# Optimization experiments

Measured on AMD Instinct MI355X. Metric: run time of the kernel, lower is better.

## Reference

```python
import jax, jax.numpy as jnp
import numpy as np

EPS = 1e-5
K_EDE, T_EDE = 1.0, 0.1  # IR-Net EDE STE params (init values); forward is pure sign


def binq(x):
    # sign binarization (forward only)
    return jnp.sign(x)


def conv3x3(x, w):
    return jax.lax.conv_general_dilated(
        x, w, window_strides=(1, 1), padding=[(1, 1), (1, 1)],
        dimension_numbers=("NCHW", "OIHW", "NCHW"))


def batchnorm(x, g, b):
    # training-mode BN: batch statistics over (N,H,W), biased variance
    mu = x.mean(axis=(0, 2, 3), keepdims=True)
    var = x.var(axis=(0, 2, 3), keepdims=True)
    return (x - mu) * jax.lax.rsqrt(var + EPS) * g.reshape(1, -1, 1, 1) + b.reshape(1, -1, 1, 1)


def maxpool2(x):
    return jax.lax.reduce_window(x, -jnp.inf, jax.lax.max,
                                 (1, 1, 2, 2), (1, 1, 2, 2), "VALID")


def hardtanh(x):
    return jnp.clip(x, -1.0, 1.0)


def skd_ir_conv(xb, xr, w):
    # IR-Net style 1W1A conv: per-out-channel standardize weights, sign-binarize
    # weights and activations; real branch uses full-precision weights, no grad.
    m = w.mean(axis=(1, 2, 3), keepdims=True)
    s = w.std(axis=(1, 2, 3), keepdims=True, ddof=1)  # torch std is unbiased
    bw = binq((w - m) / s)
    yb = conv3x3(binq(xb), bw)
    yr = jax.lax.stop_gradient(conv3x3(xr, w))
    return yb, yr


def setup_inputs() -> dict:
    key = jax.random.key(0)
    ks = jax.random.split(key, 16)

    def conv_init(k, shape):
        fan = shape[2] * shape[3] * shape[0]
        return jax.random.normal(k, shape, jnp.float32) * np.sqrt(2.0 / fan)

    d = {
        "x": jax.random.normal(ks[0], (128, 3, 32, 32), jnp.float32),
        "w0": conv_init(ks[1], (128, 3, 3, 3)),
        "w1": conv_init(ks[2], (128, 128, 3, 3)),
        "w2": conv_init(ks[3], (256, 128, 3, 3)),
        "w3": conv_init(ks[4], (256, 256, 3, 3)),
        "w4": conv_init(ks[5], (512, 256, 3, 3)),
        "w5": conv_init(ks[6], (512, 512, 3, 3)),
        "fc_w": jax.random.normal(ks[7], (10, 512 * 4 * 4), jnp.float32) * 0.01,
        "fc_b": jnp.zeros((10,), jnp.float32),
    }
    chans = [128, 128, 256, 256, 512, 512]
    for i, c in enumerate(chans):
        d[f"g{i}"] = jnp.ones((c,), jnp.float32)
        d[f"b{i}"] = jnp.zeros((c,), jnp.float32)
    return d


def reference(x, w0, w1, w2, w3, w4, w5, fc_w, fc_b,
              g0, b0, g1, b1, g2, b2, g3, b3, g4, b4, g5, b5):
    x = hardtanh(batchnorm(conv3x3(x, w0), g0, b0))

    L1b, L1r = skd_ir_conv(x, jax.lax.stop_gradient(x), w1)
    L1b = hardtanh(batchnorm(maxpool2(L1b), g1, b1))
    L1r = jax.lax.stop_gradient(hardtanh(batchnorm(maxpool2(L1r), g1, b1)))

    L2b, L2r = skd_ir_conv(L1b, L1r, w2)
    L2b = hardtanh(batchnorm(L2b, g2, b2))
    L2r = jax.lax.stop_gradient(hardtanh(batchnorm(L2r, g2, b2)))

    L3b, L3r = skd_ir_conv(L2b, L2r, w3)
    L3b = hardtanh(batchnorm(maxpool2(L3b), g3, b3))
    L3r = jax.lax.stop_gradient(hardtanh(batchnorm(maxpool2(L3r), g3, b3)))

    L4b, L4r = skd_ir_conv(L3b, L3r, w4)
    L4b = hardtanh(batchnorm(L4b, g4, b4))
    L4r = jax.lax.stop_gradient(hardtanh(batchnorm(L4r, g4, b4)))

    L5b, L5r = skd_ir_conv(L4b, L4r, w5)
    L5b = hardtanh(batchnorm(maxpool2(L5b), g5, b5))
    L5r = jax.lax.stop_gradient(hardtanh(batchnorm(maxpool2(L5r), g5, b5)))

    penul = L5b.reshape(L5b.shape[0], -1)  # [B, 512*4*4]
    out = penul @ fc_w.T + fc_b
    return (out, penul, L1b, L1r, L2b, L2r, L3b, L3r, L4b, L4r, L5b, L5r)
```

## Files before the change

### kernel.cpp

```cpp
#include <hip/hip_runtime.h>


typedef unsigned short u16;
typedef __attribute__((ext_vector_type(8))) short short8;
typedef __attribute__((ext_vector_type(8))) unsigned short ushort8;
typedef __attribute__((ext_vector_type(4))) unsigned short ushort4v;
typedef __attribute__((ext_vector_type(4))) float float4v;

__device__ __forceinline__ float bf2f(u16 u) { return __uint_as_float(((unsigned)u) << 16); }
__device__ __forceinline__ u16 f2bf(float f) {
    unsigned u = __float_as_uint(f);
    return (u16)((u + 0x7FFFu + ((u >> 16) & 1u)) >> 16);
}
__device__ __forceinline__ u16 lo_bf(float y, u16 hi) {
    return f2bf(y - bf2f(hi));
}
__device__ __forceinline__ u16 signbf(float y) {
    return y > 0.f ? 0x3F80u : (y < 0.f ? 0xBF80u : 0u);
}

__global__ __launch_bounds__(256) void conv0_main(const float* __restrict__ x,
                                                  const float* __restrict__ w0,
                                                  float* __restrict__ out) {
    __shared__ float xt[306];
    __shared__ float wl[3456];
    const int t = threadIdx.x;
    const int n = blockIdx.x >> 5;
    const int h = blockIdx.x & 31;
    for (int i = t; i < 306; i += 256) xt[i] = 0.f;
    for (int i = t; i < 3456; i += 256) wl[i] = w0[i];
    __syncthreads();
    for (int i = t; i < 288; i += 256) {
        int ci = i / 96; int rr = (i / 32) % 3; int w = i & 31;
        int gh = h - 1 + rr;
        if (gh >= 0 && gh < 32)
            xt[(ci * 3 + rr) * 34 + w + 1] = x[((n * 3 + ci) * 32 + gh) * 32 + w];
    }
    __syncthreads();
    const int w = t & 31, cg = t >> 5;
    float xin[27];
#pragma unroll
    for (int ci = 0; ci < 3; ci++)
#pragma unroll
        for (int r = 0; r < 3; r++)
#pragma unroll
            for (int kw = 0; kw < 3; kw++)
                xin[(ci * 3 + r) * 3 + kw] = xt[(ci * 3 + r) * 34 + w + kw];
    float* o = out + ((size_t)(n * 1024 + h * 32 + w)) * 128 + cg * 16;
#pragma unroll
    for (int jq = 0; jq < 4; jq++) {
        float4v v;
#pragma unroll
        for (int jk = 0; jk < 4; jk++) {
            int co = cg * 16 + jq * 4 + jk;
            float a = 0.f;
#pragma unroll
            for (int e = 0; e < 27; e++) a += xin[e] * wl[co * 27 + e];
            v[jk] = a;
        }
        *(float4v*)(o + jq * 4) = v;
    }
}

__global__ __launch_bounds__(256) void stats0_kernel(const float* __restrict__ src,
                                                     float* __restrict__ st,
                                                     int C, int rows_per_block) {
    const int t = threadIdx.x;
    const int c = blockIdx.x * 64 + (t & 63);
    const int rg = t >> 6;
    const int r0 = blockIdx.y * rows_per_block;
    float s = 0.f, q = 0.f;
    for (int r = r0 + rg; r < r0 + rows_per_block; r += 4) {
        float v = src[(size_t)r * C + c];
        s += v;
        q += v * v;
    }
    __shared__ float Ls[256], Lq[256];
    Ls[t] = s; Lq[t] = q;
    __syncthreads();
    if (t < 64) {
        s = Ls[t] + Ls[t + 64] + Ls[t + 128] + Ls[t + 192];
        q = Lq[t] + Lq[t + 64] + Lq[t + 128] + Lq[t + 192];
        atomicAdd(&st[c], s);
        atomicAdd(&st[C + c], q);
    }
}

__global__ __launch_bounds__(256) void bn0_apply(const float* __restrict__ src,
                                                 const float* __restrict__ st,
                                                 const float* __restrict__ g,
                                                 const float* __restrict__ b,
                                                 u16* __restrict__ sg,
                                                 u16* __restrict__ hi,
                                                 u16* __restrict__ lo) {
    const int t = threadIdx.x;
    __shared__ float sc[128], sh[128];
    if (t < 128) {
        float mean = st[t] * (1.f / 131072.f);
        float var = fmaxf(st[128 + t] * (1.f / 131072.f) - mean * mean, 0.f);
        float scale = rsqrtf(var + 1e-5f) * g[t];
        sc[t] = scale;
        sh[t] = b[t] - mean * scale;
    }
    __syncthreads();
    size_t i = ((size_t)blockIdx.x * 256 + t) * 4;
    int c0 = (int)(i & 127);
    float4v v = *(const float4v*)(src + i);
    ushort4v hv, lv, sv;
#pragma unroll
    for (int k = 0; k < 4; k++) {
        float y = fminf(fmaxf(v[k] * sc[c0 + k] + sh[c0 + k], -1.f), 1.f);
        hv[k] = f2bf(y);
        lv[k] = lo_bf(y, hv[k]);
        sv[k] = signbf(y);
    }
    *(ushort4v*)(sg + i) = sv;
    *(ushort4v*)(hi + i) = hv;
    *(ushort4v*)(lo + i) = lv;
}

template <bool BIN>
__global__ __launch_bounds__(256) void prepack_kernel(const float* __restrict__ w,
                                                      u16* __restrict__ apk,
                                                      u16* __restrict__ apkLo,
                                                      int Cin, int Cout) {
    const int t = threadIdx.x, o = blockIdx.x;
    const int E = Cin * 9;
    float m = 0.f;
    if (BIN) {
        float s = 0.f;
        for (int e = t; e < E; e += 256) s += w[o * E + e];
        __shared__ float Ls[256];
        Ls[t] = s;
        __syncthreads();
        for (int stp = 128; stp > 0; stp >>= 1) {
            if (t < stp) Ls[t] += Ls[t + stp];
            __syncthreads();
        }
        m = Ls[0] / (float)E;
    }
    const int CC = Cin >> 5, COT = Cout >> 7;
    for (int e = t; e < E; e += 256) {
        int ci = e / 9, tap = e % 9;
        float raw = w[o * E + e];
        int idx = ((tap * CC + (ci >> 5)) * COT + (o >> 7)) * 4096 + (o & 127) * 32 + (ci & 31);
        if (BIN) {
            apk[idx] = signbf(raw - m);
        } else {
            u16 hi = f2bf(raw);
            apk[idx] = hi;
            apkLo[idx] = lo_bf(raw, hi);
        }
    }
}

template <bool POOL, bool BIN>
__global__ __launch_bounds__(512, 2) void conv_mfma_kernel(
    const u16* __restrict__ act, const u16* __restrict__ actLo,
    const u16* __restrict__ apk, const u16* __restrict__ apkLo,
    u16* __restrict__ out, u16* __restrict__ outLo,
    int Cin, int Cout, int H, int W) {
    const int HW = H * W;
    const int t = threadIdx.x;
    const int wave = t >> 6, lane = t & 63;
    const int l15 = lane & 15, quad = lane >> 4;
    const int wm = wave >> 1, wn = wave & 1;

    const int col0 = blockIdx.x * 128;
    const int cot = blockIdx.y;
    const int CC = Cin >> 5;
    const int COT = Cout >> 7;
    const bool two = (HW < 128);
    const int Wp = W + 2;
    const int nrows = two ? 2 * (H + 2) : (128 / W + 2);
    const int n0 = col0 / HW;
    const int h0 = two ? 0 : (col0 % HW) / W;

    __shared__ __align__(16) u16 BsH[8160];
    __shared__ __align__(16) u16 BsL[BIN ? 16 : 8160];

    int bbase[4], gcol[4];
#pragma unroll
    for (int ni = 0; ni < 4; ni++) {
        int c = wn * 64 + ni * 16 + l15;
        int g = col0 + c;
        int n = g / HW; int hw = g % HW; int h = hw / W; int w = hw % W;
        gcol[ni] = g;
        int rb = two ? ((n - n0) * (H + 2) + h) : (h - h0);
        bbase[ni] = (rb * Wp + w) * 40 + quad * 8;
    }

    float4v acc[2][4];
    const float4v zf = {0.f, 0.f, 0.f, 0.f};
#pragma unroll
    for (int mi = 0; mi < 2; mi++)
#pragma unroll
        for (int ni = 0; ni < 4; ni++) acc[mi][ni] = zf;

    const int bgroups = nrows * Wp * 4;
    const size_t tapstride = (size_t)CC * COT * 4096;
    const int arow0 = wm * 1024 + l15 * 32 + quad * 8;

    short8 ahP[2][2];
    short8 alP[2][2];

    for (int cc = 0; cc < CC; cc++) {
        const u16* ab = apk + ((size_t)(cc * COT + cot)) * 4096;
        const u16* abL = apkLo + ((size_t)(cc * COT + cot)) * 4096;
#pragma unroll
        for (int mi = 0; mi < 2; mi++) {
            ahP[0][mi] = *(const short8*)(ab + arow0 + mi * 512);
            if (!BIN) alP[0][mi] = *(const short8*)(abL + arow0 + mi * 512);
        }
        __syncthreads();
#pragma unroll
        for (int j = 0; j < 2; j++) {
            int idx = t + j * 512;
            if (idx < bgroups) {
                int cig = idx & 3;
                int rest = idx >> 2;
                int wp = rest % Wp;
                int srow = rest / Wp;
                int n, gh;
                if (two) { n = n0 + srow / (H + 2); gh = srow % (H + 2) - 1; }
                else     { n = n0; gh = h0 + srow - 1; }
                int gw = wp - 1;
                short8 vh = {0, 0, 0, 0, 0, 0, 0, 0};
                short8 vl = {0, 0, 0, 0, 0, 0, 0, 0};
                if (gh >= 0 && gh < H && gw >= 0 && gw < W) {
                    size_t goff = ((size_t)(n * HW + gh * W + gw)) * Cin + cc * 32 + cig * 8;
                    vh = *(const short8*)(act + goff);
                    if (!BIN) vl = *(const short8*)(actLo + goff);
                }
                int loff = (srow * Wp + wp) * 40 + cig * 8;
                *(short8*)&BsH[loff] = vh;
                if (!BIN) *(short8*)&BsL[loff] = vl;
            }
        }
        __syncthreads();
#pragma unroll
        for (int tap = 0; tap < 9; tap++) {
            const int cur = tap & 1, nxt = cur ^ 1;
            if (tap < 8) {
                const u16* at = ab + (size_t)(tap + 1) * tapstride;
#pragma unroll
                for (int mi = 0; mi < 2; mi++)
                    ahP[nxt][mi] = *(const short8*)(at + arow0 + mi * 512);
                if (!BIN) {
                    const u16* atL = abL + (size_t)(tap + 1) * tapstride;
#pragma unroll
                    for (int mi = 0; mi < 2; mi++)
                        alP[nxt][mi] = *(const short8*)(atL + arow0 + mi * 512);
                }
            }
            const int kh = tap / 3, kw = tap % 3;
            const int boff = (kh * Wp + kw) * 40;
            short8 bh[4];
#pragma unroll
            for (int ni = 0; ni < 4; ni++)
                bh[ni] = *(const short8*)&BsH[bbase[ni] + boff];
            if (BIN) {
#pragma unroll
                for (int mi = 0; mi < 2; mi++)
#pragma unroll
                    for (int ni = 0; ni < 4; ni++)
                        acc[mi][ni] = __builtin_amdgcn_mfma_f32_16x16x32_bf16(
                            ahP[cur][mi], bh[ni], acc[mi][ni], 0, 0, 0);
            } else {
                short8 bl[4];
#pragma unroll
                for (int ni = 0; ni < 4; ni++)
                    bl[ni] = *(const short8*)&BsL[bbase[ni] + boff];
#pragma unroll
                for (int mi = 0; mi < 2; mi++)
#pragma unroll
                    for (int ni = 0; ni < 4; ni++)
                        acc[mi][ni] = __builtin_amdgcn_mfma_f32_16x16x32_bf16(
                            ahP[cur][mi], bh[ni], acc[mi][ni], 0, 0, 0);
#pragma unroll
                for (int mi = 0; mi < 2; mi++)
#pragma unroll
                    for (int ni = 0; ni < 4; ni++)
                        acc[mi][ni] = __builtin_amdgcn_mfma_f32_16x16x32_bf16(
                            ahP[cur][mi], bl[ni], acc[mi][ni], 0, 0, 0);
#pragma unroll
                for (int mi = 0; mi < 2; mi++)
#pragma unroll
                    for (int ni = 0; ni < 4; ni++)
                        acc[mi][ni] = __builtin_amdgcn_mfma_f32_16x16x32_bf16(
                            alP[cur][mi], bh[ni], acc[mi][ni], 0, 0, 0);
            }
        }
    }

    const int cobase = cot * 128 + wm * 32 + quad * 4;
    auto store4 = [&](size_t off, float4v v) {
        if (BIN) {
            ushort4v r;
#pragma unroll
            for (int k = 0; k < 4; k++) r[k] = (u16)(short)(int)v[k];
            *(ushort4v*)(out + off) = r;
        } else {
            ushort4v hi, lo;
#pragma unroll
            for (int k = 0; k < 4; k++) {
                hi[k] = f2bf(v[k]);
                lo[k] = lo_bf(v[k], hi[k]);
            }
            *(ushort4v*)(out + off) = hi;
            *(ushort4v*)(outLo + off) = lo;
        }
    };

    if (!POOL) {
#pragma unroll
        for (int mi = 0; mi < 2; mi++)
#pragma unroll
            for (int ni = 0; ni < 4; ni++)
                store4((size_t)gcol[ni] * Cout + cobase + mi * 16, acc[mi][ni]);
    } else {
        const int pH = H >> 1, pW = W >> 1;
        if (W == 32) {
#pragma unroll
            for (int mi = 0; mi < 2; mi++)
#pragma unroll
                for (int nip = 0; nip < 2; nip++) {
                    float4v v;
#pragma unroll
                    for (int k = 0; k < 4; k++)
                        v[k] = fmaxf((float)acc[mi][nip][k], (float)acc[mi][nip + 2][k]);
#pragma unroll
                    for (int k = 0; k < 4; k++) {
                        float vv = v[k];
                        v[k] = fmaxf(vv, __shfl_xor(vv, 1, 64));
                    }
                    if ((l15 & 1) == 0) {
                        int pw = nip * 8 + (l15 >> 1);
                        int ph = (h0 >> 1) + wn;
                        int prow = (n0 * pH + ph) * pW + pw;
                        store4((size_t)prow * Cout + cobase + mi * 16, v);
                    }
                }
        } else if (W == 16) {
#pragma unroll
            for (int mi = 0; mi < 2; mi++)
#pragma unroll
                for (int nip = 0; nip < 4; nip += 2) {
                    float4v v;
#pragma unroll
                    for (int k = 0; k < 4; k++)
                        v[k] = fmaxf((float)acc[mi][nip][k], (float)acc[mi][nip + 1][k]);
#pragma unroll
                    for (int k = 0; k < 4; k++) {
                        float vv = v[k];
                        v[k] = fmaxf(vv, __shfl_xor(vv, 1, 64));
                    }
                    if ((l15 & 1) == 0) {
                        int pw = l15 >> 1;
                        int ph = (h0 + wn * 4 + nip) >> 1;
                        int prow = (n0 * pH + ph) * pW + pw;
                        store4((size_t)prow * Cout + cobase + mi * 16, v);
                    }
                }
        } else {
#pragma unroll
            for (int mi = 0; mi < 2; mi++)
#pragma unroll
                for (int ni = 0; ni < 4; ni++) {
                    float4v v = acc[mi][ni];
#pragma unroll
                    for (int k = 0; k < 4; k++) {
                        float vv = v[k];
                        vv = fmaxf(vv, __shfl_xor(vv, 1, 64));
                        v[k] = fmaxf(vv, __shfl_xor(vv, 8, 64));
                    }
                    if ((l15 & 9) == 0) {
                        int pw = l15 >> 1;
                        int ph = ni;
                        int n = n0 + wn;
                        int prow = (n * pH + ph) * pW + pw;
                        store4((size_t)prow * Cout + cobase + mi * 16, v);
                    }
                }
        }
    }
}

template <bool BIN>
__global__ __launch_bounds__(256) void stats_kernel(const u16* __restrict__ src,
                                                    const u16* __restrict__ srcLo,
                                                    float* __restrict__ st,
                                                    int C, int rows_per_block) {
    const int t = threadIdx.x;
    const int c = blockIdx.x * 64 + (t & 63);
    const int rg = t >> 6;
    const int r0 = blockIdx.y * rows_per_block;
    float s = 0.f, q = 0.f;
    for (int r = r0 + rg; r < r0 + rows_per_block; r += 4) {
        size_t i = (size_t)r * C + c;
        float v = BIN ? (float)(short)src[i] : (bf2f(src[i]) + bf2f(srcLo[i]));
        s += v;
        q += v * v;
    }
    __shared__ float Ls[256], Lq[256];
    Ls[t] = s; Lq[t] = q;
    __syncthreads();
    if (t < 64) {
        s = Ls[t] + Ls[t + 64] + Ls[t + 128] + Ls[t + 192];
        q = Lq[t] + Lq[t + 64] + Lq[t + 128] + Lq[t + 192];
        atomicAdd(&st[c], s);
        atomicAdd(&st[C + c], q);
    }
}

template <bool BIN>
__global__ __launch_bounds__(256) void bn_apply_kernel(const u16* __restrict__ src,
                                                       const u16* __restrict__ srcLo,
                                                       int C, int HW,
                                                       const float* __restrict__ st, float cntinv,
                                                       const float* __restrict__ g,
                                                       const float* __restrict__ b,
                                                       float* __restrict__ dout,
                                                       float* __restrict__ dout2,
                                                       u16* __restrict__ act,
                                                       u16* __restrict__ actLo,
                                                       int act_mode) {
    const int t = threadIdx.x;
    const int cl = t & 63, rl = t >> 6;
    const int c = blockIdx.y * 64 + cl;
    const float mean = st[c] * cntinv;
    float var = st[C + c] * cntinv - mean * mean;
    var = fmaxf(var, 0.f);
    const float scale = rsqrtf(var + 1e-5f) * g[c];
    const float shift = b[c] - mean * scale;
    __shared__ float T[64][65];
#pragma unroll
    for (int i = 0; i < 16; i++) {
        int rlocal = rl + i * 4;
        int row = blockIdx.x * 64 + rlocal;
        size_t idx = (size_t)row * C + c;
        float v = BIN ? (float)(short)src[idx] : (bf2f(src[idx]) + bf2f(srcLo[idx]));
        float y = fminf(fmaxf(v * scale + shift, -1.f), 1.f);
        if (act_mode == 1) {
            u16 hi = f2bf(y);
            act[idx] = hi;
            actLo[idx] = lo_bf(y, hi);
        } else if (act_mode == 2) {
            act[idx] = signbf(y);
        }
        T[rlocal][cl] = y;
    }
    __syncthreads();
#pragma unroll
    for (int i = 0; i < 16; i++) {
        int clocal = rl + i * 4;
        int cg = blockIdx.y * 64 + clocal;
        int rglob = blockIdx.x * 64 + cl;
        int n = rglob / HW, hw = rglob % HW;
        size_t o = ((size_t)n * C + cg) * HW + hw;
        float val = T[cl][clocal];
        dout[o] = val;
        if (dout2) dout2[o] = val;
    }
}

__global__ __launch_bounds__(256) void fc_kernel(const float* __restrict__ penul,
                                                 const float* __restrict__ fcw,
                                                 const float* __restrict__ fcb,
                                                 float* __restrict__ out) {
    const int t = threadIdx.x, n = blockIdx.x;
    float acc[10];
#pragma unroll
    for (int j = 0; j < 10; j++) acc[j] = 0.f;
    for (int i = t; i < 8192; i += 256) {
        float p = penul[n * 8192 + i];
#pragma unroll
        for (int j = 0; j < 10; j++) acc[j] += p * fcw[j * 8192 + i];
    }
    __shared__ float L[10][256];
#pragma unroll
    for (int j = 0; j < 10; j++) L[j][t] = acc[j];
    __syncthreads();
    for (int s = 128; s > 0; s >>= 1) {
        if (t < s) {
#pragma unroll
            for (int j = 0; j < 10; j++) L[j][t] += L[j][t + s];
        }
        __syncthreads();
    }
    if (t < 10) out[n * 10 + t] = L[t][0] + fcb[t];
}

extern "C" void kernel_launch(void* const* d_in, const int* in_sizes, int n_in,
                              void* d_out, int out_size, void* d_ws, size_t ws_size,
                              hipStream_t stream) {
    (void)in_sizes; (void)n_in; (void)out_size; (void)ws_size;

    const float* X = (const float*)d_in[0];
    const float* W0 = (const float*)d_in[1];
    const float* Wl[5] = {(const float*)d_in[2], (const float*)d_in[3], (const float*)d_in[4],
                          (const float*)d_in[5], (const float*)d_in[6]};
    const float* FCW = (const float*)d_in[7];
    const float* FCB = (const float*)d_in[8];
    const float* G[6]; const float* Bb[6];
    for (int i = 0; i < 6; i++) { G[i] = (const float*)d_in[9 + 2 * i]; Bb[i] = (const float*)d_in[10 + 2 * i]; }

    float* OUT = (float*)d_out;
    char* ws = (char*)d_ws;

    u16* apk   = (u16*)(ws);
    u16* apkLo = (u16*)(ws + 4718592);
    float* st0 = (float*)(ws + 9437184);
    float* stk = (float*)(ws + 9439232);
    u16* F     = (u16*)(ws + 9443328);
    u16* Flo   = (u16*)(ws + 26220544);
    u16* AB    = (u16*)(ws + 42997760);
    u16* AR    = (u16*)(ws + 59774976);
    u16* ARlo  = (u16*)(ws + 76552192);

    float* C0 = (float*)(ws + 9443328);
    u16* SG   = (u16*)(OUT + 26215680);
    u16* X0   = (u16*)(OUT + 9438464);
    u16* X0lo = (u16*)(OUT + 17827072);

    float* O_out = OUT;
    float* O_pen = OUT + 1280;
    float* O_L1b = OUT + 1049856;
    float* O_L1r = OUT + 5244160;
    float* O_L2b = OUT + 9438464;
    float* O_L2r = OUT + 17827072;
    float* O_L3b = OUT + 26215680;
    float* O_L3r = OUT + 28312832;
    float* O_L4b = OUT + 30409984;
    float* O_L4r = OUT + 34604288;
    float* O_L5b = OUT + 38798592;
    float* O_L5r = OUT + 39847168;

    conv0_main<<<4096, 256, 0, stream>>>(X, W0, C0);
    hipMemsetAsync(st0, 0, 2048, stream);
    stats0_kernel<<<dim3(2, 256), 256, 0, stream>>>(C0, st0, 128, 512);
    bn0_apply<<<16384, 256, 0, stream>>>(C0, st0, G[0], Bb[0], SG, X0, X0lo);

    struct Stage {
        const float* w; int Cin, Cout, H, W; bool pool;
        dim3 cgrid; dim3 sgrid; int srpb; dim3 bgrid; int bHW; float cntinv;
        float* db; float* dr;
    };
    const Stage S[5] = {
        {Wl[0], 128, 128, 32, 32, true,  dim3(1024, 1), dim3(2, 64), 512, dim3(512, 2), 256, 1.f / 32768.f, O_L1b, O_L1r},
        {Wl[1], 128, 256, 16, 16, false, dim3(256, 2),  dim3(4, 64), 512, dim3(512, 4), 256, 1.f / 32768.f, O_L2b, O_L2r},
        {Wl[2], 256, 256, 16, 16, true,  dim3(256, 2),  dim3(4, 16), 512, dim3(128, 4), 64,  1.f / 8192.f,  O_L3b, O_L3r},
        {Wl[3], 256, 512, 8, 8,   false, dim3(64, 4),   dim3(8, 16), 512, dim3(128, 8), 64,  1.f / 8192.f,  O_L4b, O_L4r},
        {Wl[4], 512, 512, 8, 8,   true,  dim3(64, 4),   dim3(8, 16), 128, dim3(32, 8),  16,  1.f / 2048.f,  O_L5b, O_L5r},
    };

    for (int k = 0; k < 5; k++) {
        const Stage& s = S[k];
        const u16* inB = (k == 0) ? SG : AB;
        const u16* inR = (k == 0) ? X0 : AR;
        const u16* inRlo = (k == 0) ? X0lo : ARlo;

        prepack_kernel<true><<<s.Cout, 256, 0, stream>>>(s.w, apk, nullptr, s.Cin, s.Cout);
        if (s.pool) conv_mfma_kernel<true, true><<<s.cgrid, 512, 0, stream>>>(inB, nullptr, apk, apk, F, nullptr, s.Cin, s.Cout, s.H, s.W);
        else        conv_mfma_kernel<false, true><<<s.cgrid, 512, 0, stream>>>(inB, nullptr, apk, apk, F, nullptr, s.Cin, s.Cout, s.H, s.W);
        hipMemsetAsync(stk, 0, 4096, stream);
        stats_kernel<true><<<s.sgrid, 256, 0, stream>>>(F, nullptr, stk, s.Cout, s.srpb);
        bn_apply_kernel<true><<<s.bgrid, 256, 0, stream>>>(F, nullptr, s.Cout, s.bHW, stk, s.cntinv,
                                                           G[k + 1], Bb[k + 1], s.db,
                                                           (k == 4) ? O_pen : nullptr,
                                                           AB, nullptr, (k == 4) ? 0 : 2);

        prepack_kernel<false><<<s.Cout, 256, 0, stream>>>(s.w, apk, apkLo, s.Cin, s.Cout);
        if (s.pool) conv_mfma_kernel<true, false><<<s.cgrid, 512, 0, stream>>>(inR, inRlo, apk, apkLo, F, Flo, s.Cin, s.Cout, s.H, s.W);
        else        conv_mfma_kernel<false, false><<<s.cgrid, 512, 0, stream>>>(inR, inRlo, apk, apkLo, F, Flo, s.Cin, s.Cout, s.H, s.W);
        hipMemsetAsync(stk, 0, 4096, stream);
        stats_kernel<false><<<s.sgrid, 256, 0, stream>>>(F, Flo, stk, s.Cout, s.srpb);
        bn_apply_kernel<false><<<s.bgrid, 256, 0, stream>>>(F, Flo, s.Cout, s.bHW, stk, s.cntinv,
                                                            G[k + 1], Bb[k + 1], s.dr, nullptr,
                                                            AR, ARlo, (k == 4) ? 0 : 1);
    }

    fc_kernel<<<128, 256, 0, stream>>>(O_pen, FCW, FCB, O_out);
}
```

Before: 1.413 ms.

## Double-buffer shared-memory activation tiles and prefetch next channel chunk during MFMA

Doubles the LDS activation tile (hi and lo) and issues the global loads for the next 32-channel chunk, plus the first-tap weight fragments, before running the current chunk's nine taps. The loaded values are written into the alternate buffer afterwards, so each chunk needs one barrier instead of two and global latency can hide behind the MFMA work. Per-thread staging offsets are computed once outside the loop. In exchange, LDS use per block doubles in the non-binary path, which may lower occupancy, and more registers are held live for the prefetched data.

```diff
diff --git a/kernel.cpp b/kernel.cpp
--- a/kernel.cpp
+++ b/kernel.cpp
@@ -176,8 +176,8 @@
     const int n0 = col0 / HW;
     const int h0 = two ? 0 : (col0 % HW) / W;
 
-    __shared__ __align__(16) u16 BsH[8160];
-    __shared__ __align__(16) u16 BsL[BIN ? 16 : 8160];
+    __shared__ __align__(16) u16 BsH[2][8160];
+    __shared__ __align__(16) u16 BsL[BIN ? 1 : 2][BIN ? 16 : 8160];
 
     int bbase[4], gcol[4];
 #pragma unroll
@@ -190,6 +190,31 @@
         bbase[ni] = (rb * Wp + w) * 40 + quad * 8;
     }
 
+    const int bgroups = nrows * Wp * 4;
+    int svalid[2]; size_t sgoff[2]; int sloff[2];
+#pragma unroll
+    for (int j = 0; j < 2; j++) {
+        int idx = t + j * 512;
+        svalid[j] = 0; sgoff[j] = 0; sloff[j] = 0;
+        if (idx < bgroups) {
+            int cig = idx & 3;
+            int rest = idx >> 2;
+            int wp = rest % Wp;
+            int srow = rest / Wp;
+            int n, gh;
+            if (two) { n = n0 + srow / (H + 2); gh = srow % (H + 2) - 1; }
+            else     { n = n0; gh = h0 + srow - 1; }
+            int gw = wp - 1;
+            sloff[j] = (srow * Wp + wp) * 40 + cig * 8;
+            if (gh >= 0 && gh < H && gw >= 0 && gw < W) {
+                svalid[j] = 2;
+                sgoff[j] = ((size_t)(n * HW + gh * W + gw)) * Cin + cig * 8;
+            } else {
+                svalid[j] = 1;
+            }
+        }
+    }
+
     float4v acc[2][4];
     const float4v zf = {0.f, 0.f, 0.f, 0.f};
 #pragma unroll
@@ -197,60 +222,79 @@
 #pragma unroll
         for (int ni = 0; ni < 4; ni++) acc[mi][ni] = zf;
 
-    const int bgroups = nrows * Wp * 4;
     const size_t tapstride = (size_t)CC * COT * 4096;
     const int arow0 = wm * 1024 + l15 * 32 + quad * 8;
 
     short8 ahP[2][2];
     short8 alP[2][2];
+    short8 ah0N[2], al0N[2];
+    short8 svh[2], svl[2];
+    const short8 z8 = {0, 0, 0, 0, 0, 0, 0, 0};
+
+    {
+        const u16* ab0 = apk + ((size_t)cot) * 4096;
+        const u16* ab0L = apkLo + ((size_t)cot) * 4096;
+#pragma unroll
+        for (int mi = 0; mi < 2; mi++) {
+            ahP[0][mi] = *(const short8*)(ab0 + arow0 + mi * 512);
+            if (!BIN) alP[0][mi] = *(const short8*)(ab0L + arow0 + mi * 512);
+        }
+#pragma unroll
+        for (int j = 0; j < 2; j++) {
+            svh[j] = z8; svl[j] = z8;
+            if (svalid[j] == 2) {
+                svh[j] = *(const short8*)(act + sgoff[j]);
+                if (!BIN) svl[j] = *(const short8*)(actLo + sgoff[j]);
+            }
+        }
+#pragma unroll
+        for (int j = 0; j < 2; j++) {
+            if (svalid[j]) {
+                *(short8*)&BsH[0][sloff[j]] = svh[j];
+                if (!BIN) *(short8*)&BsL[0][sloff[j]] = svl[j];
+            }
+        }
+        __syncthreads();
+    }
 
     for (int cc = 0; cc < CC; cc++) {
+        const int cur = cc & 1, nx = cur ^ 1;
+        const bool more = (cc + 1 < CC);
         const u16* ab = apk + ((size_t)(cc * COT + cot)) * 4096;
         const u16* abL = apkLo + ((size_t)(cc * COT + cot)) * 4096;
-#pragma unroll
-        for (int mi = 0; mi < 2; mi++) {
-            ahP[0][mi] = *(const short8*)(ab + arow0 + mi * 512);
-            if (!BIN) alP[0][mi] = *(const short8*)(abL + arow0 + mi * 512);
-        }
-        __syncthreads();
-#pragma unroll
-        for (int j = 0; j < 2; j++) {
-            int idx = t + j * 512;
-            if (idx < bgroups) {
-                int cig = idx & 3;
-                int rest = idx >> 2;
-                int wp = rest % Wp;
-                int srow = rest / Wp;
-                int n, gh;
-                if (two) { n = n0 + srow / (H + 2); gh = srow % (H + 2) - 1; }
-                else     { n = n0; gh = h0 + srow - 1; }
-                int gw = wp - 1;
-                short8 vh = {0, 0, 0, 0, 0, 0, 0, 0};
-                short8 vl = {0, 0, 0, 0, 0, 0, 0, 0};
-                if (gh >= 0 && gh < H && gw >= 0 && gw < W) {
-                    size_t goff = ((size_t)(n * HW + gh * W + gw)) * Cin + cc * 32 + cig * 8;
-                    vh = *(const short8*)(act + goff);
-                    if (!BIN) vl = *(const short8*)(actLo + goff);
+
+        if (more) {
+            const size_t ccb = (size_t)(cc + 1) * 32;
+#pragma unroll
+            for (int j = 0; j < 2; j++) {
+                svh[j] = z8; svl[j] = z8;
+                if (svalid[j] == 2) {
+                    svh[j] = *(const short8*)(act + sgoff[j] + ccb);
+                    if (!BIN) svl[j] = *(const short8*)(actLo + sgoff[j] + ccb);
                 }
-                int loff = (srow * Wp + wp) * 40 + cig * 8;
-                *(short8*)&BsH[loff] = vh;
-                if (!BIN) *(short8*)&BsL[loff] = vl;
-            }
-        }
-        __syncthreads();
+            }
+            const u16* abN = apk + ((size_t)((cc + 1) * COT + cot)) * 4096;
+            const u16* abNL = apkLo + ((size_t)((cc + 1) * COT + cot)) * 4096;
+#pragma unroll
+            for (int mi = 0; mi < 2; mi++) {
+                ah0N[mi] = *(const short8*)(abN + arow0 + mi * 512);
+                if (!BIN) al0N[mi] = *(const short8*)(abNL + arow0 + mi * 512);
+            }
+        }
+
 #pragma unroll
         for (int tap = 0; tap < 9; tap++) {
-            const int cur = tap & 1, nxt = cur ^ 1;
+            const int curp = tap & 1, nxp = curp ^ 1;
             if (tap < 8) {
                 const u16* at = ab + (size_t)(tap + 1) * tapstride;
 #pragma unroll
                 for (int mi = 0; mi < 2; mi++)
-                    ahP[nxt][mi] = *(const short8*)(at + arow0 + mi * 512);
+                    ahP[nxp][mi] = *(const short8*)(at + arow0 + mi * 512);
                 if (!BIN) {
                     const u16* atL = abL + (size_t)(tap + 1) * tapstride;
 #pragma unroll
                     for (int mi = 0; mi < 2; mi++)
-                        alP[nxt][mi] = *(const short8*)(atL + arow0 + mi * 512);
+                        alP[nxp][mi] = *(const short8*)(atL + arow0 + mi * 512);
                 }
             }
             const int kh = tap / 3, kw = tap % 3;
@@ -258,37 +302,53 @@
             short8 bh[4];
 #pragma unroll
             for (int ni = 0; ni < 4; ni++)
-                bh[ni] = *(const short8*)&BsH[bbase[ni] + boff];
+                bh[ni] = *(const short8*)&BsH[cur][bbase[ni] + boff];
             if (BIN) {
 #pragma unroll
                 for (int mi = 0; mi < 2; mi++)
 #pragma unroll
                     for (int ni = 0; ni < 4; ni++)
                         acc[mi][ni] = __builtin_amdgcn_mfma_f32_16x16x32_bf16(
-                            ahP[cur][mi], bh[ni], acc[mi][ni], 0, 0, 0);
+                            ahP[curp][mi], bh[ni], acc[mi][ni], 0, 0, 0);
             } else {
                 short8 bl[4];
 #pragma unroll
                 for (int ni = 0; ni < 4; ni++)
-                    bl[ni] = *(const short8*)&BsL[bbase[ni] + boff];
+                    bl[ni] = *(const short8*)&BsL[cur][bbase[ni] + boff];
 #pragma unroll
                 for (int mi = 0; mi < 2; mi++)
 #pragma unroll
                     for (int ni = 0; ni < 4; ni++)
                         acc[mi][ni] = __builtin_amdgcn_mfma_f32_16x16x32_bf16(
-                            ahP[cur][mi], bh[ni], acc[mi][ni], 0, 0, 0);
+                            ahP[curp][mi], bh[ni], acc[mi][ni], 0, 0, 0);
 #pragma unroll
                 for (int mi = 0; mi < 2; mi++)
 #pragma unroll
                     for (int ni = 0; ni < 4; ni++)
                         acc[mi][ni] = __builtin_amdgcn_mfma_f32_16x16x32_bf16(
-                            ahP[cur][mi], bl[ni], acc[mi][ni], 0, 0, 0);
+                            ahP[curp][mi], bl[ni], acc[mi][ni], 0, 0, 0);
 #pragma unroll
                 for (int mi = 0; mi < 2; mi++)
 #pragma unroll
                     for (int ni = 0; ni < 4; ni++)
                         acc[mi][ni] = __builtin_amdgcn_mfma_f32_16x16x32_bf16(
-                            alP[cur][mi], bh[ni], acc[mi][ni], 0, 0, 0);
+                            alP[curp][mi], bh[ni], acc[mi][ni], 0, 0, 0);
+            }
+        }
+
+        if (more) {
+#pragma unroll
+            for (int j = 0; j < 2; j++) {
+                if (svalid[j]) {
+                    *(short8*)&BsH[nx][sloff[j]] = svh[j];
+                    if (!BIN) *(short8*)&BsL[nx][sloff[j]] = svl[j];
+                }
+            }
+            __syncthreads();
+#pragma unroll
+            for (int mi = 0; mi < 2; mi++) {
+                ahP[0][mi] = ah0N[mi];
+                if (!BIN) alP[0][mi] = al0N[mi];
             }
         }
     }
```

New measurement: 1.397 ms. Within noise of the previous version (-1.1%).
